# Kernel optimization log

Hardware: AMD Instinct MI355X
Metric: run time of the kernel (lower is better)

Reference implementation:

```python
import jax, jax.numpy as jnp
import numpy as np
from jax import lax

B, N, C = 8, 4096, 96
STRIDE, NSAMPLE, RADIUS = 4, 16, 0.1
C2 = 2 * C            # out_channels = 192 (also transfer in/out channels)
NPOINT = N // STRIDE  # 1024
EPS = 1e-5


def _fps(p, npoint):
    """Furthest point sampling. p: [B,N,3] -> idx [B,npoint] (starts at index 0)."""
    b, n, _ = p.shape
    def body(carry, _):
        mind, last = carry                       # [b,n], [b]
        lp = p[jnp.arange(b), last]              # [b,3]
        d = jnp.sum((p - lp[:, None, :]) ** 2, -1)
        mind = jnp.minimum(mind, d)
        nxt = jnp.argmax(mind, axis=1).astype(jnp.int32)
        return (mind, nxt), last
    init = (jnp.full((b, n), 1e10, p.dtype), jnp.zeros((b,), jnp.int32))
    (_, _), idxs = lax.scan(body, init, None, length=npoint)
    return jnp.transpose(idxs)                   # [b, npoint]


def _ball_query(new_p, p, radius, nsample):
    """First-nsample-in-index-order neighbors within radius; pad with first found."""
    n = p.shape[1]
    d2 = jnp.sum((new_p[:, :, None, :] - p[:, None, :, :]) ** 2, -1)  # [B,NP,N]
    order = jnp.where(d2 < radius * radius, jnp.arange(n, dtype=jnp.int32), n)
    vals, _ = lax.top_k(-order, nsample)         # k smallest 'order' values
    srt = -vals                                  # ascending valid indices, n = invalid
    return jnp.where(srt < n, srt, srt[..., :1]).astype(jnp.int32)


def _bn(y, g, b, m, v):
    """Eval-mode BatchNorm over channel axis 1."""
    shape = (1, -1) + (1,) * (y.ndim - 2)
    return (y - m.reshape(shape)) * (g.reshape(shape) / jnp.sqrt(v.reshape(shape) + EPS)) + b.reshape(shape)


def setup_inputs() -> dict:
    key = jax.random.key(0)
    ks = jax.random.split(key, 12)
    s = 1.0 / np.sqrt(C2)
    return {
        "p": jax.random.uniform(ks[0], (B, N, 3), jnp.float32),
        "x": jax.random.normal(ks[1], (B, C, N), jnp.float32),
        "Wt": jax.random.normal(ks[2], (C2, C2), jnp.float32) * s,
        "gt": 1.0 + 0.1 * jax.random.normal(ks[3], (C2,), jnp.float32),
        "bt": 0.1 * jax.random.normal(ks[4], (C2,), jnp.float32),
        "mt": 0.1 * jax.random.normal(ks[5], (C2,), jnp.float32),
        "vt": jax.random.uniform(ks[6], (C2,), jnp.float32, 0.5, 1.5),
        "Wc": jax.random.normal(ks[7], (C2, C2), jnp.float32) * s,
        "gc": 1.0 + 0.1 * jax.random.normal(ks[8], (C2,), jnp.float32),
        "bc": 0.1 * jax.random.normal(ks[9], (C2,), jnp.float32),
        "mc": 0.1 * jax.random.normal(ks[10], (C2,), jnp.float32),
        "vc": jax.random.uniform(ks[11], (C2,), jnp.float32, 0.5, 1.5),
    }


def reference(p, x, Wt, gt, bt, mt, vt, Wc, gc, bc, mc, vc):
    b = p.shape[0]
    bidx = jnp.arange(b)[:, None]
    # --- FPS sample + gather centers ---
    samp = _fps(p, NPOINT)                       # [B,NP]
    new_p = p[bidx, samp]                        # [B,NP,3]
    # --- ball-query grouping ---
    nbr = _ball_query(new_p, p, RADIUS, NSAMPLE)  # [B,NP,NS]
    bidx2 = jnp.arange(b)[:, None, None]
    gp = p[bidx2, nbr]                           # [B,NP,NS,3]
    dp = jnp.transpose(gp - new_p[:, :, None, :], (0, 3, 1, 2))  # [B,3,NP,NS]
    xt = jnp.transpose(x, (0, 2, 1))             # [B,N,C]
    gx = jnp.transpose(xt[bidx2, nbr], (0, 3, 1, 2))             # [B,C,NP,NS]
    cx = jnp.transpose(xt[bidx, samp], (0, 2, 1))[..., None]     # [B,C,NP,1]
    xj = jnp.concatenate([jnp.broadcast_to(cx, gx.shape), gx], axis=1)  # [B,2C,NP,NS]
    # --- act + transfer (1x1 conv + BN + relu) ---
    xj = jax.nn.relu(xj)
    xj = jax.nn.relu(_bn(jnp.einsum('oc,bcgs->bogs', Wt, xj), gt, bt, mt, vt))
    # --- PosPool sin/cos positional encoding ---
    fd = C2 // 6
    dim_mat = jnp.float32(500.0) ** (jnp.arange(fd, dtype=jnp.float32) / fd)
    pos = (50.0 * dp)[..., None] / dim_mat       # [B,3,NP,NS,fd]
    emb = jnp.concatenate([jnp.sin(pos), jnp.cos(pos)], -1)      # [B,3,NP,NS,2fd]
    emb = jnp.transpose(emb, (0, 1, 4, 2, 3)).reshape(xj.shape)  # [B,C2,NP,NS]
    agg = xj * emb + emb
    # --- max + mean pool over neighbors ---
    pooled = jnp.max(agg, -1) + jnp.mean(agg, -1)                # [B,C2,NP]
    # --- act + convs (1x1 conv + BN + relu) ---
    out = jax.nn.relu(_bn(jnp.einsum('oc,bcg->bog', Wc, jax.nn.relu(pooled)), gc, bc, mc, vc))
    return new_p, out
```

## Files before the change

kernel.cpp:

```cpp
#include <hip/hip_runtime.h>
#include <math.h>

#define BB 8
#define NN 4096
#define CC 96
#define C2 192
#define NP 1024
#define NS 16
#define PPT 16

#define SAMP_OFF   0u
#define NBR_OFF    32768u
#define WSW_OFF    655360u
#define B1_OFF     802816u
#define WCT_OFF    803584u
#define B2_OFF     951040u
#define ZT_OFF     958464u

__global__ __launch_bounds__(256) void fps_prep_kernel(
        const float* __restrict__ p,
        const float* __restrict__ Wt, const float* __restrict__ gt,
        const float* __restrict__ bt, const float* __restrict__ mt,
        const float* __restrict__ vt, const float* __restrict__ Wc,
        const float* __restrict__ gc, const float* __restrict__ bc,
        const float* __restrict__ mc, const float* __restrict__ vc,
        float* __restrict__ Ws, float* __restrict__ beta1,
        float* __restrict__ WcT, float* __restrict__ beta2,
        int* __restrict__ samp, float* __restrict__ out) {
    if (blockIdx.x >= BB) {
        int i = (blockIdx.x - BB) * 256 + threadIdx.x;
        if (i < C2) {
            float s1 = gt[i] / sqrtf(vt[i] + 1e-5f);
            beta1[i] = bt[i] - mt[i] * s1;
            float s2 = gc[i] / sqrtf(vc[i] + 1e-5f);
            beta2[i] = bc[i] - mc[i] * s2;
        }
        if (i < 384 * 96) {
            int r = i / 96, c = i - r * 96;
            int o = (r < C2) ? r : r - C2;
            float s1 = gt[o] / sqrtf(vt[o] + 1e-5f);
            float w = (r < C2) ? Wt[o * C2 + c] : Wt[o * C2 + 96 + c];
            Ws[i] = w * s1;
        }
        if (i < C2 * C2) {
            int o = i / C2, c = i - o * C2;
            float s2 = gc[o] / sqrtf(vc[o] + 1e-5f);
            WcT[c * C2 + o] = Wc[i] * s2;
        }
        return;
    }
    int b = blockIdx.x;
    const float* pb = p + (size_t)b * NN * 3;
    __shared__ float sx[NN], sy[NN], sz[NN];
    __shared__ unsigned long long redk[2][4];
    int tid = threadIdx.x;

    float px[PPT], py[PPT], pz[PPT], mind[PPT];
    int jbase = tid * PPT;
    for (int i = 0; i < PPT; ++i) {
        int j = jbase + i;
        float a = pb[j * 3 + 0];
        float c = pb[j * 3 + 1];
        float d = pb[j * 3 + 2];
        px[i] = a; py[i] = c; pz[i] = d;
        mind[i] = 1e10f;
        sx[j] = a; sy[j] = c; sz[j] = d;
    }
    __syncthreads();

    int last = 0;
    float lx = sx[0], ly = sy[0], lz = sz[0];
    unsigned inv_base = 4095u - (unsigned)jbase;

    for (int it = 0; it < NP; ++it) {
        if (tid == 0) {
            samp[b * NP + it] = last;
            size_t o3 = ((size_t)b * NP + it) * 3;
            out[o3 + 0] = lx; out[o3 + 1] = ly; out[o3 + 2] = lz;
        }
        unsigned long long key = 0ull;
        #pragma unroll
        for (int i = 0; i < PPT; ++i) {
            float dx = __fsub_rn(px[i], lx);
            float dy = __fsub_rn(py[i], ly);
            float dz = __fsub_rn(pz[i], lz);
            float d = __fadd_rn(__fadd_rn(__fmul_rn(dx, dx), __fmul_rn(dy, dy)),
                                __fmul_rn(dz, dz));
            float m = fminf(mind[i], d);
            mind[i] = m;
            unsigned long long k =
                ((unsigned long long)__float_as_uint(m) << 32) | (unsigned long long)(inv_base - i);
            key = (k > key) ? k : key;
        }
        #pragma unroll
        for (int off = 1; off < 64; off <<= 1) {
            unsigned long long o = __shfl_xor(key, off, 64);
            key = (o > key) ? o : key;
        }
        if ((tid & 63) == 0) redk[it & 1][tid >> 6] = key;
        __syncthreads();
        unsigned long long k0 = redk[it & 1][0], k1 = redk[it & 1][1];
        unsigned long long k2 = redk[it & 1][2], k3 = redk[it & 1][3];
        k0 = (k1 > k0) ? k1 : k0;
        k2 = (k3 > k2) ? k3 : k2;
        k0 = (k2 > k0) ? k2 : k0;
        int bi = 4095 - (int)(unsigned)(k0 & 0xffffffffull);
        last = bi;
        lx = sx[bi]; ly = sy[bi]; lz = sz[bi];
    }
}

__global__ __launch_bounds__(256) void bq_gemm_kernel(
        const float* __restrict__ p, const float* __restrict__ newp,
        int* __restrict__ nbr,
        const float* __restrict__ x, const float* __restrict__ Ws,
        float* __restrict__ zt) {
    __shared__ float smem[12352];
    int tid = threadIdx.x;

    if (blockIdx.x < 2048) {
        float* sx = smem;
        float* sy = smem + NN;
        float* sz = smem + 2 * NN;
        int blk = blockIdx.x;
        int b = blk >> 8;
        const float* pb = p + (size_t)b * NN * 3;
        for (int idx = tid; idx < NN; idx += 256) {
            sx[idx] = pb[idx * 3 + 0];
            sy[idx] = pb[idx * 3 + 1];
            sz[idx] = pb[idx * 3 + 2];
        }
        __syncthreads();
        int wave = tid >> 6, lane = tid & 63;
        int g = (blk & 255) * 4 + wave;
        int gidx = b * NP + g;
        float cx = newp[(size_t)gidx * 3 + 0];
        float cy = newp[(size_t)gidx * 3 + 1];
        float cz = newp[(size_t)gidx * 3 + 2];
        const float R2 = 0.01f;
        int cnt = 0, first = -1;
        for (int chunk = 0; chunk < NN / 64 && cnt < NS; ++chunk) {
            int j = chunk * 64 + lane;
            float dx = __fsub_rn(cx, sx[j]);
            float dy = __fsub_rn(cy, sy[j]);
            float dz = __fsub_rn(cz, sz[j]);
            float d2 = __fadd_rn(__fadd_rn(__fmul_rn(dx, dx), __fmul_rn(dy, dy)),
                                 __fmul_rn(dz, dz));
            unsigned long long mask = __ballot(d2 < R2);
            while (mask && cnt < NS) {
                int bit = __ffsll(mask) - 1;
                mask &= mask - 1;
                int idx = chunk * 64 + bit;
                if (first < 0) first = idx;
                if (lane == 0) nbr[(size_t)gidx * NS + cnt] = idx;
                ++cnt;
            }
        }
        if (lane == 0) {
            for (int i = cnt; i < NS; ++i) nbr[(size_t)gidx * NS + i] = first;
        }
    } else {
        float* xt = smem;
        float* wt = smem + 6144;
        int g = blockIdx.x - 2048;
        int b = g & 7;
        int t2 = g >> 3;
        int ob = t2 >> 6;
        int jt = t2 & 63;

        for (int idx = tid; idx < 96 * 64; idx += 256) {
            int c = idx >> 6, j = idx & 63;
            xt[c * 64 + j] = fmaxf(x[((size_t)b * CC + c) * NN + jt * 64 + j], 0.0f);
        }
        for (int idx = tid; idx < 64 * 96; idx += 256) {
            int r = idx / 96, c = idx - r * 96;
            wt[r * 97 + c] = Ws[(ob * 64 + r) * 96 + c];
        }
        __syncthreads();

        int ty = tid >> 4, tx = tid & 15;
        float acc[4][4] = {};
        for (int k = 0; k < 96; ++k) {
            float a0 = wt[(ty * 4 + 0) * 97 + k];
            float a1 = wt[(ty * 4 + 1) * 97 + k];
            float a2 = wt[(ty * 4 + 2) * 97 + k];
            float a3 = wt[(ty * 4 + 3) * 97 + k];
            float4 bv = *(const float4*)&xt[k * 64 + tx * 4];
            acc[0][0] = fmaf(a0, bv.x, acc[0][0]); acc[0][1] = fmaf(a0, bv.y, acc[0][1]);
            acc[0][2] = fmaf(a0, bv.z, acc[0][2]); acc[0][3] = fmaf(a0, bv.w, acc[0][3]);
            acc[1][0] = fmaf(a1, bv.x, acc[1][0]); acc[1][1] = fmaf(a1, bv.y, acc[1][1]);
            acc[1][2] = fmaf(a1, bv.z, acc[1][2]); acc[1][3] = fmaf(a1, bv.w, acc[1][3]);
            acc[2][0] = fmaf(a2, bv.x, acc[2][0]); acc[2][1] = fmaf(a2, bv.y, acc[2][1]);
            acc[2][2] = fmaf(a2, bv.z, acc[2][2]); acc[2][3] = fmaf(a2, bv.w, acc[2][3]);
            acc[3][0] = fmaf(a3, bv.x, acc[3][0]); acc[3][1] = fmaf(a3, bv.y, acc[3][1]);
            acc[3][2] = fmaf(a3, bv.z, acc[3][2]); acc[3][3] = fmaf(a3, bv.w, acc[3][3]);
        }
        for (int jj = 0; jj < 4; ++jj) {
            int j = jt * 64 + tx * 4 + jj;
            float4 v = make_float4(acc[0][jj], acc[1][jj], acc[2][jj], acc[3][jj]);
            *(float4*)&zt[((size_t)b * NN + j) * 384 + ob * 64 + ty * 4] = v;
        }
    }
}

__global__ __launch_bounds__(192) void fused_kernel(const float* __restrict__ p,
                                                    const float* __restrict__ newp,
                                                    const int* __restrict__ samp,
                                                    const int* __restrict__ nbr,
                                                    const float* __restrict__ zt,
                                                    const float* __restrict__ beta1,
                                                    const float* __restrict__ WcT,
                                                    const float* __restrict__ beta2,
                                                    float* __restrict__ out) {
    int blk = blockIdx.x;
    int b = blk >> 10, g = blk & 1023;
    int tid = threadIdx.x;
    __shared__ float dp[3][NS];
    __shared__ int nb[NS];
    __shared__ float pl[C2];

    if (tid < NS) {
        int j = nbr[(size_t)blk * NS + tid];
        nb[tid] = j;
        dp[0][tid] = p[((size_t)b * NN + j) * 3 + 0] - newp[(size_t)blk * 3 + 0];
        dp[1][tid] = p[((size_t)b * NN + j) * 3 + 1] - newp[(size_t)blk * 3 + 1];
        dp[2][tid] = p[((size_t)b * NN + j) * 3 + 2] - newp[(size_t)blk * 3 + 2];
    }
    __syncthreads();

    int o = tid;
    int sidx = samp[blk];
    float zc = zt[((size_t)b * NN + sidx) * 384 + o];
    float bet = beta1[o];
    int axis = o >> 6;
    int k = o & 63;
    int kk = (k < 32) ? k : k - 32;
    float dim = powf(500.0f, (float)kk * (1.0f / 32.0f));

    float mx = -3.4e38f, sm = 0.0f;
    for (int s = 0; s < NS; ++s) {
        float zn = zt[((size_t)b * NN + nb[s]) * 384 + C2 + o];
        float t = fmaxf(zc + zn + bet, 0.0f);
        float pos = (50.0f * dp[axis][s]) / dim;
        float e = (k < 32) ? sinf(pos) : cosf(pos);
        float a = fmaf(t, e, e);
        mx = fmaxf(mx, a);
        sm += a;
    }
    pl[o] = fmaxf(mx + sm * (1.0f / 16.0f), 0.0f);
    __syncthreads();

    float acc = 0.0f;
    for (int c = 0; c < C2; ++c) acc = fmaf(WcT[c * C2 + o], pl[c], acc);
    float res = fmaxf(acc + beta2[o], 0.0f);
    out[BB * NP * 3 + ((size_t)b * C2 + o) * NP + g] = res;
}

extern "C" void kernel_launch(void* const* d_in, const int* in_sizes, int n_in,
                              void* d_out, int out_size, void* d_ws, size_t ws_size,
                              hipStream_t stream) {
    (void)in_sizes; (void)n_in; (void)out_size; (void)ws_size;
    const float* p  = (const float*)d_in[0];
    const float* x  = (const float*)d_in[1];
    const float* Wt = (const float*)d_in[2];
    const float* gt = (const float*)d_in[3];
    const float* bt = (const float*)d_in[4];
    const float* mt = (const float*)d_in[5];
    const float* vt = (const float*)d_in[6];
    const float* Wc = (const float*)d_in[7];
    const float* gc = (const float*)d_in[8];
    const float* bc = (const float*)d_in[9];
    const float* mc = (const float*)d_in[10];
    const float* vc = (const float*)d_in[11];
    float* out = (float*)d_out;
    char* ws = (char*)d_ws;

    int*   samp  = (int*)(ws + SAMP_OFF);
    int*   nbr   = (int*)(ws + NBR_OFF);
    float* Ws    = (float*)(ws + WSW_OFF);
    float* beta1 = (float*)(ws + B1_OFF);
    float* WcT   = (float*)(ws + WCT_OFF);
    float* beta2 = (float*)(ws + B2_OFF);
    float* zt    = (float*)(ws + ZT_OFF);
    const float* newp = out;

    fps_prep_kernel<<<dim3(BB + 145), dim3(256), 0, stream>>>(
        p, Wt, gt, bt, mt, vt, Wc, gc, bc, mc, vc,
        Ws, beta1, WcT, beta2, samp, out);
    bq_gemm_kernel<<<dim3(2048 + 3072), dim3(256), 0, stream>>>(
        p, newp, nbr, x, Ws, zt);
    fused_kernel<<<dim3(BB * NP), dim3(192), 0, stream>>>(
        p, newp, samp, nbr, zt, beta1, WcT, beta2, out);
}
```

Measured before the change: 974.1 us.

## Speed up FPS argmax loop with packed math, float argmax and DPP reduction

Rewrites the furthest-point-sampling inner loop. Distances are computed with two-wide packed float vectors, and each thread picks its local maximum with a float compare tree instead of 64-bit key compares. The wavefront reduction uses DPP row shifts and row broadcasts instead of xor shuffles. Point loads are vectorised to float4, and the shared-memory coordinate arrays are merged into an xy float2 array plus a z array. This targets per-iteration latency on the serial 1024-step chain. It relies on the GFX9 DPP broadcast controls and on strict comparisons to keep lowest-index tie-breaking.

```diff
diff --git a/kernel.cpp b/kernel.cpp
--- a/kernel.cpp
+++ b/kernel.cpp
@@ -9,6 +9,8 @@
 #define NS 16
 #define PPT 16
 
+typedef float v2f __attribute__((ext_vector_type(2)));
+
 #define SAMP_OFF   0u
 #define NBR_OFF    32768u
 #define WSW_OFF    655360u
@@ -16,6 +18,15 @@
 #define WCT_OFF    803584u
 #define B2_OFF     951040u
 #define ZT_OFF     958464u
+
+template<int CTRL, int RM>
+__device__ __forceinline__ unsigned long long dpp_mov64(unsigned long long k) {
+    int tlo = __builtin_amdgcn_update_dpp(0, (int)(unsigned)(k & 0xffffffffull),
+                                          CTRL, RM, 0xf, false);
+    int thi = __builtin_amdgcn_update_dpp(0, (int)(unsigned)(k >> 32),
+                                          CTRL, RM, 0xf, false);
+    return ((unsigned long long)(unsigned)thi << 32) | (unsigned)tlo;
+}
 
 __global__ __launch_bounds__(256) void fps_prep_kernel(
         const float* __restrict__ p,
@@ -49,28 +60,35 @@
         }
         return;
     }
+    {
+#pragma clang fp contract(off)
     int b = blockIdx.x;
     const float* pb = p + (size_t)b * NN * 3;
-    __shared__ float sx[NN], sy[NN], sz[NN];
+    __shared__ float2 sxy[NN];
+    __shared__ float  szz[NN];
     __shared__ unsigned long long redk[2][4];
     int tid = threadIdx.x;
-
-    float px[PPT], py[PPT], pz[PPT], mind[PPT];
     int jbase = tid * PPT;
-    for (int i = 0; i < PPT; ++i) {
-        int j = jbase + i;
-        float a = pb[j * 3 + 0];
-        float c = pb[j * 3 + 1];
-        float d = pb[j * 3 + 2];
-        px[i] = a; py[i] = c; pz[i] = d;
-        mind[i] = 1e10f;
-        sx[j] = a; sy[j] = c; sz[j] = d;
-    }
-    __syncthreads();
+
+    float c48[48];
+    const float4* pb4 = (const float4*)(pb + (size_t)jbase * 3);
+    #pragma unroll
+    for (int i = 0; i < 12; ++i) ((float4*)c48)[i] = pb4[i];
+    v2f px2[8], py2[8], pz2[8], mind2[8];
+    #pragma unroll
+    for (int q = 0; q < 8; ++q) {
+        px2[q].x = c48[6*q+0]; px2[q].y = c48[6*q+3];
+        py2[q].x = c48[6*q+1]; py2[q].y = c48[6*q+4];
+        pz2[q].x = c48[6*q+2]; pz2[q].y = c48[6*q+5];
+        mind2[q].x = 1e10f;    mind2[q].y = 1e10f;
+        sxy[jbase + 2*q]     = make_float2(c48[6*q+0], c48[6*q+1]);
+        szz[jbase + 2*q]     = c48[6*q+2];
+        sxy[jbase + 2*q + 1] = make_float2(c48[6*q+3], c48[6*q+4]);
+        szz[jbase + 2*q + 1] = c48[6*q+5];
+    }
 
     int last = 0;
-    float lx = sx[0], ly = sy[0], lz = sz[0];
-    unsigned inv_base = 4095u - (unsigned)jbase;
+    float lx = pb[0], ly = pb[1], lz = pb[2];
 
     for (int it = 0; it < NP; ++it) {
         if (tid == 0) {
@@ -78,26 +96,58 @@
             size_t o3 = ((size_t)b * NP + it) * 3;
             out[o3 + 0] = lx; out[o3 + 1] = ly; out[o3 + 2] = lz;
         }
-        unsigned long long key = 0ull;
+        v2f lx2; lx2.x = lx; lx2.y = lx;
+        v2f ly2; ly2.x = ly; ly2.y = ly;
+        v2f lz2; lz2.x = lz; lz2.y = lz;
+        float m[16];
         #pragma unroll
-        for (int i = 0; i < PPT; ++i) {
-            float dx = __fsub_rn(px[i], lx);
-            float dy = __fsub_rn(py[i], ly);
-            float dz = __fsub_rn(pz[i], lz);
-            float d = __fadd_rn(__fadd_rn(__fmul_rn(dx, dx), __fmul_rn(dy, dy)),
-                                __fmul_rn(dz, dz));
-            float m = fminf(mind[i], d);
-            mind[i] = m;
-            unsigned long long k =
-                ((unsigned long long)__float_as_uint(m) << 32) | (unsigned long long)(inv_base - i);
-            key = (k > key) ? k : key;
-        }
+        for (int q = 0; q < 8; ++q) {
+            v2f dx = px2[q] - lx2;
+            v2f dy = py2[q] - ly2;
+            v2f dz = pz2[q] - lz2;
+            v2f dd = (dx * dx + dy * dy) + dz * dz;
+            float m0 = fminf(mind2[q].x, dd.x);
+            float m1 = fminf(mind2[q].y, dd.y);
+            mind2[q].x = m0; mind2[q].y = m1;
+            m[2*q] = m0; m[2*q+1] = m1;
+        }
+        float v8[8]; int i8v[8];
         #pragma unroll
-        for (int off = 1; off < 64; off <<= 1) {
-            unsigned long long o = __shfl_xor(key, off, 64);
-            key = (o > key) ? o : key;
-        }
-        if ((tid & 63) == 0) redk[it & 1][tid >> 6] = key;
+        for (int q = 0; q < 8; ++q) {
+            bool t = m[2*q+1] > m[2*q];
+            v8[q] = t ? m[2*q+1] : m[2*q];
+            i8v[q] = t ? 2*q+1 : 2*q;
+        }
+        float v4[4]; int i4v[4];
+        #pragma unroll
+        for (int q = 0; q < 4; ++q) {
+            bool t = v8[2*q+1] > v8[2*q];
+            v4[q] = t ? v8[2*q+1] : v8[2*q];
+            i4v[q] = t ? i8v[2*q+1] : i8v[2*q];
+        }
+        float v2a[2]; int i2v[2];
+        #pragma unroll
+        for (int q = 0; q < 2; ++q) {
+            bool t = v4[2*q+1] > v4[2*q];
+            v2a[q] = t ? v4[2*q+1] : v4[2*q];
+            i2v[q] = t ? i4v[2*q+1] : i4v[2*q];
+        }
+        bool tf = v2a[1] > v2a[0];
+        float bv = tf ? v2a[1] : v2a[0];
+        int ii  = tf ? i2v[1] : i2v[0];
+        unsigned long long key =
+            ((unsigned long long)__float_as_uint(bv) << 32)
+            | (unsigned)(4095 - (jbase + ii));
+
+        unsigned long long t;
+        t = dpp_mov64<0x111, 0xf>(key); key = (t > key) ? t : key;
+        t = dpp_mov64<0x112, 0xf>(key); key = (t > key) ? t : key;
+        t = dpp_mov64<0x114, 0xf>(key); key = (t > key) ? t : key;
+        t = dpp_mov64<0x118, 0xf>(key); key = (t > key) ? t : key;
+        t = dpp_mov64<0x142, 0xa>(key); key = (t > key) ? t : key;
+        t = dpp_mov64<0x143, 0xc>(key); key = (t > key) ? t : key;
+
+        if ((tid & 63) == 63) redk[it & 1][tid >> 6] = key;
         __syncthreads();
         unsigned long long k0 = redk[it & 1][0], k1 = redk[it & 1][1];
         unsigned long long k2 = redk[it & 1][2], k3 = redk[it & 1][3];
@@ -106,7 +156,9 @@
         k0 = (k2 > k0) ? k2 : k0;
         int bi = 4095 - (int)(unsigned)(k0 & 0xffffffffull);
         last = bi;
-        lx = sx[bi]; ly = sy[bi]; lz = sz[bi];
+        float2 xy = sxy[bi];
+        lx = xy.x; ly = xy.y; lz = szz[bi];
+    }
     }
 }
 
```

New measurement: 971.1 us. About the same (-0.3%).

## Rework FPS reduction with DPP wave max and 512 threads carrying coordinates

Applied to the files above, without the earlier changes.

The furthest-point-sampling loop now runs 512 threads with 8 points each instead of 256 with 16. The per-wave argmax uses DPP row shifts and broadcasts plus a readlane in place of a shuffle butterfly. The winning point's coordinates travel with the key through the cross-wave LDS reduction, so the shared-memory copy of all points is no longer needed. The aim is to cut latency on each of the 1024 serial iterations, at the cost of 8 waves synchronising per iteration instead of 4. Point loads become float4 vector loads, and the prep blocks are resized to match.

```diff
diff --git a/kernel.cpp b/kernel.cpp
--- a/kernel.cpp
+++ b/kernel.cpp
@@ -7,7 +7,7 @@
 #define C2 192
 #define NP 1024
 #define NS 16
-#define PPT 16
+#define FPT 8
 
 #define SAMP_OFF   0u
 #define NBR_OFF    32768u
@@ -17,7 +17,16 @@
 #define B2_OFF     951040u
 #define ZT_OFF     958464u
 
-__global__ __launch_bounds__(256) void fps_prep_kernel(
+template<int CTRL, int RM>
+__device__ __forceinline__ unsigned long long dpp_mov64(unsigned long long k) {
+    int tlo = __builtin_amdgcn_update_dpp(0, (int)(unsigned)(k & 0xffffffffull),
+                                          CTRL, RM, 0xf, false);
+    int thi = __builtin_amdgcn_update_dpp(0, (int)(unsigned)(k >> 32),
+                                          CTRL, RM, 0xf, false);
+    return ((unsigned long long)(unsigned)thi << 32) | (unsigned)tlo;
+}
+
+__global__ __launch_bounds__(512) void fps_prep_kernel(
         const float* __restrict__ p,
         const float* __restrict__ Wt, const float* __restrict__ gt,
         const float* __restrict__ bt, const float* __restrict__ mt,
@@ -28,7 +37,7 @@
         float* __restrict__ WcT, float* __restrict__ beta2,
         int* __restrict__ samp, float* __restrict__ out) {
     if (blockIdx.x >= BB) {
-        int i = (blockIdx.x - BB) * 256 + threadIdx.x;
+        int i = (blockIdx.x - BB) * 512 + threadIdx.x;
         if (i < C2) {
             float s1 = gt[i] / sqrtf(vt[i] + 1e-5f);
             beta1[i] = bt[i] - mt[i] * s1;
@@ -51,25 +60,24 @@
     }
     int b = blockIdx.x;
     const float* pb = p + (size_t)b * NN * 3;
-    __shared__ float sx[NN], sy[NN], sz[NN];
-    __shared__ unsigned long long redk[2][4];
+    __shared__ unsigned long long redk[2][8];
+    __shared__ float4 redc[2][8];
     int tid = threadIdx.x;
-
-    float px[PPT], py[PPT], pz[PPT], mind[PPT];
-    int jbase = tid * PPT;
-    for (int i = 0; i < PPT; ++i) {
-        int j = jbase + i;
-        float a = pb[j * 3 + 0];
-        float c = pb[j * 3 + 1];
-        float d = pb[j * 3 + 2];
-        px[i] = a; py[i] = c; pz[i] = d;
+    int jbase = tid * FPT;
+
+    float c24[24];
+    const float4* pb4 = (const float4*)(pb + (size_t)jbase * 3);
+    #pragma unroll
+    for (int i = 0; i < 6; ++i) ((float4*)c24)[i] = pb4[i];
+    float px[FPT], py[FPT], pz[FPT], mind[FPT];
+    #pragma unroll
+    for (int i = 0; i < FPT; ++i) {
+        px[i] = c24[3*i+0]; py[i] = c24[3*i+1]; pz[i] = c24[3*i+2];
         mind[i] = 1e10f;
-        sx[j] = a; sy[j] = c; sz[j] = d;
-    }
-    __syncthreads();
+    }
 
     int last = 0;
-    float lx = sx[0], ly = sy[0], lz = sz[0];
+    float lx = pb[0], ly = pb[1], lz = pb[2];
     unsigned inv_base = 4095u - (unsigned)jbase;
 
     for (int it = 0; it < NP; ++it) {
@@ -78,35 +86,76 @@
             size_t o3 = ((size_t)b * NP + it) * 3;
             out[o3 + 0] = lx; out[o3 + 1] = ly; out[o3 + 2] = lz;
         }
-        unsigned long long key = 0ull;
+        float m[FPT];
         #pragma unroll
-        for (int i = 0; i < PPT; ++i) {
+        for (int i = 0; i < FPT; ++i) {
             float dx = __fsub_rn(px[i], lx);
             float dy = __fsub_rn(py[i], ly);
             float dz = __fsub_rn(pz[i], lz);
             float d = __fadd_rn(__fadd_rn(__fmul_rn(dx, dx), __fmul_rn(dy, dy)),
                                 __fmul_rn(dz, dz));
-            float m = fminf(mind[i], d);
-            mind[i] = m;
-            unsigned long long k =
-                ((unsigned long long)__float_as_uint(m) << 32) | (unsigned long long)(inv_base - i);
-            key = (k > key) ? k : key;
-        }
+            float mi = fminf(mind[i], d);
+            mind[i] = mi;
+            m[i] = mi;
+        }
+        float v4[4]; int i4v[4];
         #pragma unroll
-        for (int off = 1; off < 64; off <<= 1) {
-            unsigned long long o = __shfl_xor(key, off, 64);
-            key = (o > key) ? o : key;
-        }
-        if ((tid & 63) == 0) redk[it & 1][tid >> 6] = key;
+        for (int q = 0; q < 4; ++q) {
+            bool t = m[2*q+1] > m[2*q];
+            v4[q] = t ? m[2*q+1] : m[2*q];
+            i4v[q] = t ? 2*q+1 : 2*q;
+        }
+        float v2a[2]; int i2v[2];
+        #pragma unroll
+        for (int q = 0; q < 2; ++q) {
+            bool t = v4[2*q+1] > v4[2*q];
+            v2a[q] = t ? v4[2*q+1] : v4[2*q];
+            i2v[q] = t ? i4v[2*q+1] : i4v[2*q];
+        }
+        bool tf = v2a[1] > v2a[0];
+        float bv = tf ? v2a[1] : v2a[0];
+        int ii  = tf ? i2v[1] : i2v[0];
+        unsigned long long key =
+            ((unsigned long long)__float_as_uint(bv) << 32)
+            | (unsigned long long)(inv_base - (unsigned)ii);
+
+        unsigned long long red = key, t;
+        t = dpp_mov64<0x111, 0xf>(red); red = (t > red) ? t : red;
+        t = dpp_mov64<0x112, 0xf>(red); red = (t > red) ? t : red;
+        t = dpp_mov64<0x114, 0xf>(red); red = (t > red) ? t : red;
+        t = dpp_mov64<0x118, 0xf>(red); red = (t > red) ? t : red;
+        t = dpp_mov64<0x142, 0xa>(red); red = (t > red) ? t : red;
+        t = dpp_mov64<0x143, 0xc>(red); red = (t > red) ? t : red;
+
+        unsigned rlo = (unsigned)__builtin_amdgcn_readlane((int)(unsigned)(red & 0xffffffffull), 63);
+        unsigned rhi = (unsigned)__builtin_amdgcn_readlane((int)(unsigned)(red >> 32), 63);
+        unsigned long long wkey = ((unsigned long long)rhi << 32) | rlo;
+        int buf = it & 1;
+        if (key == wkey) {
+            int wv = tid >> 6;
+            redk[buf][wv] = wkey;
+            redc[buf][wv] = make_float4(px[ii], py[ii], pz[ii], 0.0f);
+        }
         __syncthreads();
-        unsigned long long k0 = redk[it & 1][0], k1 = redk[it & 1][1];
-        unsigned long long k2 = redk[it & 1][2], k3 = redk[it & 1][3];
-        k0 = (k1 > k0) ? k1 : k0;
-        k2 = (k3 > k2) ? k3 : k2;
-        k0 = (k2 > k0) ? k2 : k0;
-        int bi = 4095 - (int)(unsigned)(k0 & 0xffffffffull);
-        last = bi;
-        lx = sx[bi]; ly = sy[bi]; lz = sz[bi];
+
+        unsigned long long k0 = redk[buf][0], k1 = redk[buf][1];
+        unsigned long long k2 = redk[buf][2], k3 = redk[buf][3];
+        unsigned long long k4 = redk[buf][4], k5 = redk[buf][5];
+        unsigned long long k6 = redk[buf][6], k7 = redk[buf][7];
+        float4 c0 = redc[buf][0], c1 = redc[buf][1];
+        float4 c2 = redc[buf][2], c3 = redc[buf][3];
+        float4 c4 = redc[buf][4], c5 = redc[buf][5];
+        float4 c6 = redc[buf][6], c7 = redc[buf][7];
+        #define MRG(ka, ca, kb, cb) { bool tm = (kb) > (ka); \
+            ka = tm ? (kb) : (ka); \
+            ca.x = tm ? cb.x : ca.x; ca.y = tm ? cb.y : ca.y; ca.z = tm ? cb.z : ca.z; }
+        MRG(k0, c0, k1, c1); MRG(k2, c2, k3, c3);
+        MRG(k4, c4, k5, c5); MRG(k6, c6, k7, c7);
+        MRG(k0, c0, k2, c2); MRG(k4, c4, k6, c6);
+        MRG(k0, c0, k4, c4);
+        #undef MRG
+        last = 4095 - (int)(unsigned)(k0 & 0xffffffffull);
+        lx = c0.x; ly = c0.y; lz = c0.z;
     }
 }
 
@@ -284,7 +333,7 @@
     float* zt    = (float*)(ws + ZT_OFF);
     const float* newp = out;
 
-    fps_prep_kernel<<<dim3(BB + 145), dim3(256), 0, stream>>>(
+    fps_prep_kernel<<<dim3(BB + 72), dim3(512), 0, stream>>>(
         p, Wt, gt, bt, mt, vt, Wc, gc, bc, mc, vc,
         Ws, beta1, WcT, beta2, samp, out);
     bq_gemm_kernel<<<dim3(2048 + 3072), dim3(256), 0, stream>>>(
```

Measured after the change: 1.198 ms. 23.0% more time.

## Interleave two FPS batches per block with DPP argmax and coordinate broadcast

Applied to the files above, without the earlier changes.

The furthest-point-sampling kernel now handles two batches per block and interleaves their scans so each iteration has more independent work to hide latency. The 64-bit key shuffle reduction is replaced by a local tree argmax, a DPP float max and a ballot to pick the winning lane. The winner's coordinates are passed through shared memory, so the shared-memory point copy is no longer needed. The BN-scaled transfer weight is now folded inside the GEMM blocks instead of in a prep kernel. FPS now runs on only 4 blocks, which halves its parallelism, and the per-iteration sync work per block grows.

```diff
diff --git a/kernel.cpp b/kernel.cpp
--- a/kernel.cpp
+++ b/kernel.cpp
@@ -11,37 +11,88 @@
 
 #define SAMP_OFF   0u
 #define NBR_OFF    32768u
-#define WSW_OFF    655360u
 #define B1_OFF     802816u
 #define WCT_OFF    803584u
 #define B2_OFF     951040u
 #define ZT_OFF     958464u
 
+template<int CTRL, int RM>
+__device__ __forceinline__ float dpp_maxf(float v) {
+    int t = __builtin_amdgcn_update_dpp(0, __float_as_int(v), CTRL, RM, 0xf, false);
+    return fmaxf(v, __int_as_float(t));
+}
+
+#define SCAN_ARGMAX(px, py, pz, mind, lx, ly, lz, bv, ii) {                  \
+    float m[PPT];                                                            \
+    _Pragma("unroll")                                                        \
+    for (int i = 0; i < PPT; ++i) {                                          \
+        float dx = __fsub_rn(px[i], lx);                                     \
+        float dy = __fsub_rn(py[i], ly);                                     \
+        float dz = __fsub_rn(pz[i], lz);                                     \
+        float d = __fadd_rn(__fadd_rn(__fmul_rn(dx, dx), __fmul_rn(dy, dy)), \
+                            __fmul_rn(dz, dz));                              \
+        float mi = fminf(mind[i], d);                                        \
+        mind[i] = mi; m[i] = mi;                                             \
+    }                                                                        \
+    float v8[8]; int i8v[8];                                                 \
+    _Pragma("unroll")                                                        \
+    for (int q = 0; q < 8; ++q) {                                            \
+        bool t = m[2*q+1] > m[2*q];                                          \
+        v8[q] = t ? m[2*q+1] : m[2*q];                                       \
+        i8v[q] = t ? 2*q+1 : 2*q;                                            \
+    }                                                                        \
+    float v4[4]; int i4v[4];                                                 \
+    _Pragma("unroll")                                                        \
+    for (int q = 0; q < 4; ++q) {                                            \
+        bool t = v8[2*q+1] > v8[2*q];                                        \
+        v4[q] = t ? v8[2*q+1] : v8[2*q];                                     \
+        i4v[q] = t ? i8v[2*q+1] : i8v[2*q];                                  \
+    }                                                                        \
+    float v2a[2]; int i2v[2];                                                \
+    _Pragma("unroll")                                                        \
+    for (int q = 0; q < 2; ++q) {                                            \
+        bool t = v4[2*q+1] > v4[2*q];                                        \
+        v2a[q] = t ? v4[2*q+1] : v4[2*q];                                    \
+        i2v[q] = t ? i4v[2*q+1] : i4v[2*q];                                  \
+    }                                                                        \
+    bool tf = v2a[1] > v2a[0];                                               \
+    bv = tf ? v2a[1] : v2a[0];                                               \
+    ii = tf ? i2v[1] : i2v[0];                                               \
+}
+
+#define DPP_REDUCE(r) {                       \
+    r = dpp_maxf<0x111, 0xf>(r);              \
+    r = dpp_maxf<0x112, 0xf>(r);              \
+    r = dpp_maxf<0x114, 0xf>(r);              \
+    r = dpp_maxf<0x118, 0xf>(r);              \
+    r = dpp_maxf<0x142, 0xa>(r);              \
+    r = dpp_maxf<0x143, 0xc>(r);              \
+}
+
+#define MRG(ka, ca, kb, cb) { bool tm = (kb) > (ka);                          \
+    ka = tm ? (kb) : (ka);                                                    \
+    ca.x = tm ? cb.x : ca.x; ca.y = tm ? cb.y : ca.y; ca.z = tm ? cb.z : ca.z; }
+
 __global__ __launch_bounds__(256) void fps_prep_kernel(
         const float* __restrict__ p,
-        const float* __restrict__ Wt, const float* __restrict__ gt,
-        const float* __restrict__ bt, const float* __restrict__ mt,
-        const float* __restrict__ vt, const float* __restrict__ Wc,
-        const float* __restrict__ gc, const float* __restrict__ bc,
-        const float* __restrict__ mc, const float* __restrict__ vc,
-        float* __restrict__ Ws, float* __restrict__ beta1,
-        float* __restrict__ WcT, float* __restrict__ beta2,
+        const float* __restrict__ gt, const float* __restrict__ bt,
+        const float* __restrict__ mt, const float* __restrict__ vt,
+        const float* __restrict__ Wc, const float* __restrict__ gc,
+        const float* __restrict__ bc, const float* __restrict__ mc,
+        const float* __restrict__ vc,
+        float* __restrict__ beta1, float* __restrict__ WcT,
+        float* __restrict__ beta2,
         int* __restrict__ samp, float* __restrict__ out) {
-    if (blockIdx.x >= BB) {
-        int i = (blockIdx.x - BB) * 256 + threadIdx.x;
+    int tid = threadIdx.x;
+
+    if (blockIdx.x >= 4) {
+        int i = (blockIdx.x - 4) * 256 + tid;
         if (i < C2) {
             float s1 = gt[i] / sqrtf(vt[i] + 1e-5f);
             beta1[i] = bt[i] - mt[i] * s1;
             float s2 = gc[i] / sqrtf(vc[i] + 1e-5f);
             beta2[i] = bc[i] - mc[i] * s2;
         }
-        if (i < 384 * 96) {
-            int r = i / 96, c = i - r * 96;
-            int o = (r < C2) ? r : r - C2;
-            float s1 = gt[o] / sqrtf(vt[o] + 1e-5f);
-            float w = (r < C2) ? Wt[o * C2 + c] : Wt[o * C2 + 96 + c];
-            Ws[i] = w * s1;
-        }
         if (i < C2 * C2) {
             int o = i / C2, c = i - o * C2;
             float s2 = gc[o] / sqrtf(vc[o] + 1e-5f);
@@ -49,73 +100,103 @@
         }
         return;
     }
-    int b = blockIdx.x;
-    const float* pb = p + (size_t)b * NN * 3;
-    __shared__ float sx[NN], sy[NN], sz[NN];
-    __shared__ unsigned long long redk[2][4];
-    int tid = threadIdx.x;
-
-    float px[PPT], py[PPT], pz[PPT], mind[PPT];
+
+    int b0 = blockIdx.x << 1;
+    const float* pbA = p + (size_t)b0 * NN * 3;
+    const float* pbB = pbA + NN * 3;
+    __shared__ unsigned long long redk[2][2][4];
+    __shared__ float4 redc[2][2][4];
     int jbase = tid * PPT;
+
+    float c48[48];
+    const float4* pA4 = (const float4*)(pbA + (size_t)jbase * 3);
+    #pragma unroll
+    for (int i = 0; i < 12; ++i) ((float4*)c48)[i] = pA4[i];
+    float pxA[PPT], pyA[PPT], pzA[PPT], mindA[PPT];
+    #pragma unroll
     for (int i = 0; i < PPT; ++i) {
-        int j = jbase + i;
-        float a = pb[j * 3 + 0];
-        float c = pb[j * 3 + 1];
-        float d = pb[j * 3 + 2];
-        px[i] = a; py[i] = c; pz[i] = d;
-        mind[i] = 1e10f;
-        sx[j] = a; sy[j] = c; sz[j] = d;
-    }
-    __syncthreads();
-
-    int last = 0;
-    float lx = sx[0], ly = sy[0], lz = sz[0];
-    unsigned inv_base = 4095u - (unsigned)jbase;
+        pxA[i] = c48[3*i+0]; pyA[i] = c48[3*i+1]; pzA[i] = c48[3*i+2];
+        mindA[i] = 1e10f;
+    }
+    const float4* pB4 = (const float4*)(pbB + (size_t)jbase * 3);
+    #pragma unroll
+    for (int i = 0; i < 12; ++i) ((float4*)c48)[i] = pB4[i];
+    float pxB[PPT], pyB[PPT], pzB[PPT], mindB[PPT];
+    #pragma unroll
+    for (int i = 0; i < PPT; ++i) {
+        pxB[i] = c48[3*i+0]; pyB[i] = c48[3*i+1]; pzB[i] = c48[3*i+2];
+        mindB[i] = 1e10f;
+    }
+
+    int lastA = 0, lastB = 0;
+    float lxA = pbA[0], lyA = pbA[1], lzA = pbA[2];
+    float lxB = pbB[0], lyB = pbB[1], lzB = pbB[2];
 
     for (int it = 0; it < NP; ++it) {
         if (tid == 0) {
-            samp[b * NP + it] = last;
-            size_t o3 = ((size_t)b * NP + it) * 3;
-            out[o3 + 0] = lx; out[o3 + 1] = ly; out[o3 + 2] = lz;
-        }
-        unsigned long long key = 0ull;
-        #pragma unroll
-        for (int i = 0; i < PPT; ++i) {
-            float dx = __fsub_rn(px[i], lx);
-            float dy = __fsub_rn(py[i], ly);
-            float dz = __fsub_rn(pz[i], lz);
-            float d = __fadd_rn(__fadd_rn(__fmul_rn(dx, dx), __fmul_rn(dy, dy)),
-                                __fmul_rn(dz, dz));
-            float m = fminf(mind[i], d);
-            mind[i] = m;
-            unsigned long long k =
-                ((unsigned long long)__float_as_uint(m) << 32) | (unsigned long long)(inv_base - i);
-            key = (k > key) ? k : key;
-        }
-        #pragma unroll
-        for (int off = 1; off < 64; off <<= 1) {
-            unsigned long long o = __shfl_xor(key, off, 64);
-            key = (o > key) ? o : key;
-        }
-        if ((tid & 63) == 0) redk[it & 1][tid >> 6] = key;
+            samp[b0 * NP + it] = lastA;
+            samp[(b0 + 1) * NP + it] = lastB;
+            size_t oA = ((size_t)b0 * NP + it) * 3;
+            out[oA + 0] = lxA; out[oA + 1] = lyA; out[oA + 2] = lzA;
+            size_t oB = ((size_t)(b0 + 1) * NP + it) * 3;
+            out[oB + 0] = lxB; out[oB + 1] = lyB; out[oB + 2] = lzB;
+        }
+        float bvA; int iiA;
+        SCAN_ARGMAX(pxA, pyA, pzA, mindA, lxA, lyA, lzA, bvA, iiA);
+        float bvB; int iiB;
+        SCAN_ARGMAX(pxB, pyB, pzB, mindB, lxB, lyB, lzB, bvB, iiB);
+
+        float rA = bvA; DPP_REDUCE(rA);
+        float rB = bvB; DPP_REDUCE(rB);
+        float wmaxA = __int_as_float(__builtin_amdgcn_readlane(__float_as_int(rA), 63));
+        float wmaxB = __int_as_float(__builtin_amdgcn_readlane(__float_as_int(rB), 63));
+
+        unsigned long long ballA = __ballot(bvA == wmaxA);
+        unsigned long long ballB = __ballot(bvB == wmaxB);
+        int winA = (int)(__ffsll((long long)ballA) - 1);
+        int winB = (int)(__ffsll((long long)ballB) - 1);
+        int buf = it & 1;
+        int wv = tid >> 6, lane = tid & 63;
+        if (lane == winA) {
+            redk[buf][0][wv] = ((unsigned long long)__float_as_uint(bvA) << 32)
+                               | (unsigned long long)(unsigned)(4095 - (jbase + iiA));
+            redc[buf][0][wv] = make_float4(pxA[iiA], pyA[iiA], pzA[iiA], 0.0f);
+        }
+        if (lane == winB) {
+            redk[buf][1][wv] = ((unsigned long long)__float_as_uint(bvB) << 32)
+                               | (unsigned long long)(unsigned)(4095 - (jbase + iiB));
+            redc[buf][1][wv] = make_float4(pxB[iiB], pyB[iiB], pzB[iiB], 0.0f);
+        }
         __syncthreads();
-        unsigned long long k0 = redk[it & 1][0], k1 = redk[it & 1][1];
-        unsigned long long k2 = redk[it & 1][2], k3 = redk[it & 1][3];
-        k0 = (k1 > k0) ? k1 : k0;
-        k2 = (k3 > k2) ? k3 : k2;
-        k0 = (k2 > k0) ? k2 : k0;
-        int bi = 4095 - (int)(unsigned)(k0 & 0xffffffffull);
-        last = bi;
-        lx = sx[bi]; ly = sy[bi]; lz = sz[bi];
+
+        {
+            unsigned long long k0 = redk[buf][0][0], k1 = redk[buf][0][1];
+            unsigned long long k2 = redk[buf][0][2], k3 = redk[buf][0][3];
+            float4 c0 = redc[buf][0][0], c1 = redc[buf][0][1];
+            float4 c2 = redc[buf][0][2], c3 = redc[buf][0][3];
+            MRG(k0, c0, k1, c1); MRG(k2, c2, k3, c3); MRG(k0, c0, k2, c2);
+            lastA = 4095 - (int)(unsigned)(k0 & 0xffffffffull);
+            lxA = c0.x; lyA = c0.y; lzA = c0.z;
+        }
+        {
+            unsigned long long k0 = redk[buf][1][0], k1 = redk[buf][1][1];
+            unsigned long long k2 = redk[buf][1][2], k3 = redk[buf][1][3];
+            float4 c0 = redc[buf][1][0], c1 = redc[buf][1][1];
+            float4 c2 = redc[buf][1][2], c3 = redc[buf][1][3];
+            MRG(k0, c0, k1, c1); MRG(k2, c2, k3, c3); MRG(k0, c0, k2, c2);
+            lastB = 4095 - (int)(unsigned)(k0 & 0xffffffffull);
+            lxB = c0.x; lyB = c0.y; lzB = c0.z;
+        }
     }
 }
 
 __global__ __launch_bounds__(256) void bq_gemm_kernel(
         const float* __restrict__ p, const float* __restrict__ newp,
         int* __restrict__ nbr,
-        const float* __restrict__ x, const float* __restrict__ Ws,
+        const float* __restrict__ x, const float* __restrict__ Wt,
+        const float* __restrict__ gt, const float* __restrict__ vt,
         float* __restrict__ zt) {
-    __shared__ float smem[12352];
+    __shared__ float smem[12416];
     int tid = threadIdx.x;
 
     if (blockIdx.x < 2048) {
@@ -162,19 +243,28 @@
     } else {
         float* xt = smem;
         float* wt = smem + 6144;
+        float* s1s = smem + 12352;
         int g = blockIdx.x - 2048;
         int b = g & 7;
         int t2 = g >> 3;
         int ob = t2 >> 6;
         int jt = t2 & 63;
 
+        if (tid < 64) {
+            int grow = ob * 64 + tid;
+            int o = (grow < C2) ? grow : grow - C2;
+            s1s[tid] = gt[o] / sqrtf(vt[o] + 1e-5f);
+        }
         for (int idx = tid; idx < 96 * 64; idx += 256) {
             int c = idx >> 6, j = idx & 63;
             xt[c * 64 + j] = fmaxf(x[((size_t)b * CC + c) * NN + jt * 64 + j], 0.0f);
         }
+        __syncthreads();
         for (int idx = tid; idx < 64 * 96; idx += 256) {
             int r = idx / 96, c = idx - r * 96;
-            wt[r * 97 + c] = Ws[(ob * 64 + r) * 96 + c];
+            int grow = ob * 64 + r;
+            float w = (grow < C2) ? Wt[grow * C2 + c] : Wt[(grow - C2) * C2 + 96 + c];
+            wt[r * 97 + c] = w * s1s[r];
         }
         __syncthreads();
 
@@ -277,18 +367,17 @@
 
     int*   samp  = (int*)(ws + SAMP_OFF);
     int*   nbr   = (int*)(ws + NBR_OFF);
-    float* Ws    = (float*)(ws + WSW_OFF);
     float* beta1 = (float*)(ws + B1_OFF);
     float* WcT   = (float*)(ws + WCT_OFF);
     float* beta2 = (float*)(ws + B2_OFF);
     float* zt    = (float*)(ws + ZT_OFF);
     const float* newp = out;
 
-    fps_prep_kernel<<<dim3(BB + 145), dim3(256), 0, stream>>>(
-        p, Wt, gt, bt, mt, vt, Wc, gc, bc, mc, vc,
-        Ws, beta1, WcT, beta2, samp, out);
+    fps_prep_kernel<<<dim3(4 + 144), dim3(256), 0, stream>>>(
+        p, gt, bt, mt, vt, Wc, gc, bc, mc, vc,
+        beta1, WcT, beta2, samp, out);
     bq_gemm_kernel<<<dim3(2048 + 3072), dim3(256), 0, stream>>>(
-        p, newp, nbr, x, Ws, zt);
+        p, newp, nbr, x, Wt, gt, vt, zt);
     fused_kernel<<<dim3(BB * NP), dim3(192), 0, stream>>>(
         p, newp, samp, nbr, zt, beta1, WcT, beta2, out);
 }
```

Result: slower. 2.672 ms (+174.3%).
